# Kernel tuning notes

Hardware: AMD Instinct MI355X
Metric: run time of the kernel (lower is better)

The kernel has to match this reference:

```python
import jax, jax.numpy as jnp
from jax import lax
import numpy as np

NDIM = 256
BATCH = 65536
NROT = NDIM * (NDIM - 1) // 2  # comb(ndim, 2) = 32640


def _givens_mat(rots, ii, jj, ndim):
    """Product G_last @ ... @ G_1 of Givens rotations in combinations order.

    Left-multiplying by G(i, j, theta) only modifies rows i and j, so we apply
    each rotation as a rank-2 row update instead of a full matmul (same math
    as the original `plane_rot_mat @ mat` loop).
    """
    def step(mat, carry):
        i, j, th = carry
        c = jnp.cos(th)
        s = jnp.sin(th)
        ri = mat[i]
        rj = mat[j]
        mat = mat.at[i].set(c * ri - s * rj)
        mat = mat.at[j].set(s * ri + c * rj)
        return mat, None

    mat0 = jnp.eye(ndim, dtype=jnp.complex64)
    mat, _ = lax.scan(step, mat0, (ii, jj, rots))
    return mat


def setup_inputs() -> dict:
    key = jax.random.key(0)
    k1, k2, k3, k4 = jax.random.split(key, 4)
    x = jax.random.normal(k1, (BATCH, NDIM), dtype=jnp.float32)
    rots1 = 0.1 * jax.random.normal(k2, (NROT,), dtype=jnp.float32)
    phases = 0.1 * jax.random.normal(k3, (NDIM,), dtype=jnp.float32)
    rots2 = 0.1 * jax.random.normal(k4, (NROT,), dtype=jnp.float32)
    return {"x": x, "rots1": rots1, "phases": phases, "rots2": rots2}


def reference(x, rots1, phases, rots2):
    ndim = x.shape[1]
    # np.triu_indices(ndim, 1) enumerates (i, j) pairs in the same row-major
    # order as itertools.combinations(range(ndim), 2).
    ii_np, jj_np = np.triu_indices(ndim, k=1)
    ii = jnp.asarray(ii_np, dtype=jnp.int32)
    jj = jnp.asarray(jj_np, dtype=jnp.int32)

    # vector_norm: row-wise L2 normalization
    xn = x / jnp.linalg.norm(x, axis=1, keepdims=True)
    xc = xn.astype(jnp.complex64)

    # rot1: y = x @ M1.T with M1 = G_last @ ... @ G_1
    M1 = _givens_mat(rots1, ii, jj, ndim)
    y = xc @ M1.T

    # phase_transforms: x @ diag(exp(i*phases)) == elementwise phase multiply
    y = y * jnp.exp(1j * phases)

    # rot2
    M2 = _givens_mat(rots2, ii, jj, ndim)
    y = y @ M2.T

    # measure: |.|^2
    return jnp.abs(y) ** 2
```

## Files before the change

kernel.cpp:

```cpp
#include <hip/hip_runtime.h>
#include <stdint.h>
#include <math.h>

#define NDIM 256
#define BATCH 65536
#define NROT 32640

typedef float  f32x4 __attribute__((ext_vector_type(4)));
typedef short  s16x8 __attribute__((ext_vector_type(8)));
typedef unsigned int u32x4 __attribute__((ext_vector_type(4)));
typedef unsigned int u32x2 __attribute__((ext_vector_type(2)));

static __device__ __forceinline__ unsigned short f2bf(float f) {
    unsigned int u = __float_as_uint(f);
    u += 0x7fffu + ((u >> 16) & 1u);
    return (unsigned short)(u >> 16);
}
static __device__ __forceinline__ float bf2f(unsigned short h) {
    return __uint_as_float(((unsigned)h) << 16);
}

static __device__ __forceinline__ void split4(f32x4 v, u32x2* hi, u32x2* lo) {
    unsigned short h[4], l[4];
    #pragma unroll
    for (int i = 0; i < 4; i++) {
        h[i] = f2bf(v[i]);
        l[i] = f2bf(v[i] - bf2f(h[i]));
    }
    *hi = (u32x2){ (unsigned)h[0] | ((unsigned)h[1] << 16),
                   (unsigned)h[2] | ((unsigned)h[3] << 16) };
    *lo = (u32x2){ (unsigned)l[0] | ((unsigned)l[1] << 16),
                   (unsigned)l[2] | ((unsigned)l[3] << 16) };
}
static __device__ __forceinline__ void split8(const float* v, u32x4* hi, u32x4* lo) {
    unsigned short h[8], l[8];
    #pragma unroll
    for (int i = 0; i < 8; i++) {
        h[i] = f2bf(v[i]);
        l[i] = f2bf(v[i] - bf2f(h[i]));
    }
    *hi = (u32x4){ (unsigned)h[0] | ((unsigned)h[1] << 16),
                   (unsigned)h[2] | ((unsigned)h[3] << 16),
                   (unsigned)h[4] | ((unsigned)h[5] << 16),
                   (unsigned)h[6] | ((unsigned)h[7] << 16) };
    *lo = (u32x4){ (unsigned)l[0] | ((unsigned)l[1] << 16),
                   (unsigned)l[2] | ((unsigned)l[3] << 16),
                   (unsigned)l[4] | ((unsigned)l[5] << 16),
                   (unsigned)l[6] | ((unsigned)l[7] << 16) };
}

static __device__ __forceinline__ int sweep_bound(int k, int pblk) {
    int target = k * (NROT / pblk);
    int best = 0, bd = 0x7fffffff;
    for (int i = 0; i <= 256; i += 4) {
        int pre = i * 255 - (i * (i - 1)) / 2;
        int d = pre - target; d = (d < 0) ? -d : d;
        if (d < bd) { bd = d; best = i; }
    }
    return best;
}

__global__ __launch_bounds__(256) void k_cs(const float* __restrict__ r1,
                                            const float* __restrict__ r2,
                                            float2* __restrict__ cs) {
    int i = blockIdx.x * 256 + threadIdx.x;
    float th = (i < NROT) ? r1[i] : r2[i - NROT];
    float sv, cv; sincosf(th, &sv, &cv);
    cs[i] = make_float2(cv, sv);
}

__global__ __launch_bounds__(64) void k_blocks(const float2* __restrict__ cs,
                                               float* __restrict__ bmats, int pblk) {
    __shared__ float colb[264 * 64];
    __shared__ float2 csb[256 * 4];
    __shared__ float2 tri[24 * 6];

    const int t = threadIdx.x;
    const int bid = blockIdx.x;
    const int chunk = bid & 3;
    const int b = (bid >> 2) % pblk;
    const int set = (bid >> 2) / pblk;
    const int col0 = chunk * 64;
    const float2* cst = cs + (size_t)set * NROT;

    const int s0 = sweep_bound(b, pblk);
    const int s1 = sweep_bound(b + 1, pblk);
    const int ngroups = (s1 - s0) >> 2;

    {
        const f32x4 z = {0.f, 0.f, 0.f, 0.f};
        #pragma unroll 11
        for (int q = 0; q < 66; q++)
            *(f32x4*)&colb[(q * 64 + t) * 4] = z;
        colb[(col0 + t) * 64 + t] = 1.0f;
    }

    for (int k = t; k < ngroups * 6; k += 64) {
        int g = k / 6, q = k - g * 6;
        int a  = (q < 3) ? 0 : ((q < 5) ? 1 : 2);
        int bb = (q < 3) ? (q + 1) : ((q < 5) ? (q - 1) : 3);
        int m0 = s0 + g * 4;
        int m = m0 + a;
        int base = m * 255 - (m * (m - 1)) / 2;
        tri[k] = cst[base - m - 1 + m0 + bb];
    }

    float2 gv[16];
    {
        const int m0g = s0;
        int offg[4];
        #pragma unroll
        for (int a = 0; a < 4; a++) {
            int m = m0g + a;
            offg[a] = m * 255 - (m * (m - 1)) / 2 - m - 1;
        }
        #pragma unroll
        for (int it = 0; it < 16; it++) {
            int k = t + it * 64;
            int jj = k >> 2, a = k & 3;
            int j = m0g + 4 + jj;
            gv[it] = (j < 256) ? cst[offg[a] + j] : make_float2(1.f, 0.f);
        }
        #pragma unroll
        for (int it = 0; it < 16; it++)
            csb[t + it * 64] = gv[it];
    }

    for (int g = 0; g < ngroups; g++) {
        const int m0 = s0 + g * 4;
        const int n_j = 252 - m0;
        const int n_p = (n_j > 0) ? ((n_j + 7) & ~7) : 0;
        const float* csbuf = (const float*)&csb[0];

        const bool have_next = (g + 1 < ngroups);
        if (have_next) {
            const int m0g = m0 + 4;
            int offg[4];
            #pragma unroll
            for (int a = 0; a < 4; a++) {
                int m = m0g + a;
                offg[a] = m * 255 - (m * (m - 1)) / 2 - m - 1;
            }
            #pragma unroll
            for (int it = 0; it < 16; it++) {
                int k = t + it * 64;
                int jj = k >> 2, a = k & 3;
                int j = m0g + 4 + jj;
                gv[it] = (j < 256) ? cst[offg[a] + j] : make_float2(1.f, 0.f);
            }
        }

        float u0 = colb[(m0 + 0) * 64 + t];
        float u1 = colb[(m0 + 1) * 64 + t];
        float u2 = colb[(m0 + 2) * 64 + t];
        float u3 = colb[(m0 + 3) * 64 + t];

        {
            float2 cv; float nr;
            cv = tri[g * 6 + 0]; nr = cv.y * u0 + cv.x * u1; u0 = cv.x * u0 - cv.y * u1; u1 = nr;
            cv = tri[g * 6 + 1]; nr = cv.y * u0 + cv.x * u2; u0 = cv.x * u0 - cv.y * u2; u2 = nr;
            cv = tri[g * 6 + 2]; nr = cv.y * u0 + cv.x * u3; u0 = cv.x * u0 - cv.y * u3; u3 = nr;
            cv = tri[g * 6 + 3]; nr = cv.y * u1 + cv.x * u2; u1 = cv.x * u1 - cv.y * u2; u2 = nr;
            cv = tri[g * 6 + 4]; nr = cv.y * u1 + cv.x * u3; u1 = cv.x * u1 - cv.y * u3; u3 = nr;
            cv = tri[g * 6 + 5]; nr = cv.y * u2 + cv.x * u3; u2 = cv.x * u2 - cv.y * u3; u3 = nr;
        }

        if (n_p > 0) {
            float rbuf[8];
            f32x4 abuf[8][2];
            #pragma unroll
            for (int p = 0; p < 8; p++) {
                rbuf[p] = colb[(m0 + 4 + p) * 64 + t];
                abuf[p][0] = *(const f32x4*)&csbuf[p * 8 + 0];
                abuf[p][1] = *(const f32x4*)&csbuf[p * 8 + 4];
            }
            for (int c = 0; c < n_p; c += 8) {
                #pragma unroll
                for (int p = 0; p < 8; p++) {
                    const int j = m0 + 4 + c + p;
                    float r = rbuf[p];
                    f32x4 A01 = abuf[p][0], A23 = abuf[p][1];
                    int jn = j + 8; jn = (jn < 263) ? jn : 263;
                    int cn = c + p + 8; cn = (cn < n_p) ? cn : (n_p - 1);
                    rbuf[p] = colb[jn * 64 + t];
                    abuf[p][0] = *(const f32x4*)&csbuf[cn * 8 + 0];
                    abuf[p][1] = *(const f32x4*)&csbuf[cn * 8 + 4];
                    float nr;
                    nr = A01[1] * u0 + A01[0] * r; u0 = A01[0] * u0 - A01[1] * r; r = nr;
                    nr = A01[3] * u1 + A01[2] * r; u1 = A01[2] * u1 - A01[3] * r; r = nr;
                    nr = A23[1] * u2 + A23[0] * r; u2 = A23[0] * u2 - A23[1] * r; r = nr;
                    nr = A23[3] * u3 + A23[2] * r; u3 = A23[2] * u3 - A23[3] * r; r = nr;
                    colb[j * 64 + t] = r;
                }
            }
        }
        colb[(m0 + 0) * 64 + t] = u0;
        colb[(m0 + 1) * 64 + t] = u1;
        colb[(m0 + 2) * 64 + t] = u2;
        colb[(m0 + 3) * 64 + t] = u3;

        if (have_next) {
            #pragma unroll
            for (int it = 0; it < 16; it++)
                csb[t + it * 64] = gv[it];
        }
    }

    float* outm = bmats + (size_t)(set * pblk + b) * 65536;
    for (int r = 0; r < 256; r++)
        outm[(size_t)r * 256 + col0 + t] = colb[r * 64 + t];
}

static __device__ __forceinline__ void xnorm_item(const float* __restrict__ xg,
                                                  unsigned short* __restrict__ xbf,
                                                  int id, int tid) {
    const int w = tid >> 6, lane = tid & 63;
    const int r0 = id * 64;
    #pragma unroll 2
    for (int p = 0; p < 16; p++) {
        int row = r0 + p * 4 + w;
        f32x4 v = *(const f32x4*)&xg[(size_t)row * 256 + lane * 4];
        float s = v[0] * v[0] + v[1] * v[1] + v[2] * v[2] + v[3] * v[3];
        #pragma unroll
        for (int off = 32; off; off >>= 1) s += __shfl_xor(s, off, 64);
        float sc = 1.0f / sqrtf(s);
        unsigned short h0 = f2bf(v[0] * sc), h1 = f2bf(v[1] * sc);
        unsigned short h2 = f2bf(v[2] * sc), h3 = f2bf(v[3] * sc);
        u32x2 pk = { (unsigned)h0 | ((unsigned)h1 << 16),
                     (unsigned)h2 | ((unsigned)h3 << 16) };
        *(u32x2*)&xbf[(size_t)row * 256 + lane * 4] = pk;
    }
}

#define TB 2560

static __device__ __forceinline__ void tile_issueA(const float* __restrict__ Am,
                                                   int tr, int kb, int tid,
                                                   f32x4 va[2]) {
    #pragma unroll
    for (int it = 0; it < 2; it++) {
        int flat = tid + it * 256;
        int r = flat >> 3, c4 = flat & 7;
        va[it] = *(const f32x4*)&Am[(size_t)(tr * 64 + r) * 256 + kb * 32 + c4 * 4];
    }
}
static __device__ __forceinline__ void tile_issueB(const float* __restrict__ Bm,
                                                   int tc, int kb, int bn, int bkq,
                                                   float vb[8]) {
    #pragma unroll
    for (int i = 0; i < 8; i++)
        vb[i] = Bm[(size_t)(kb * 32 + bkq * 8 + i) * 256 + tc * 64 + bn];
}
static __device__ __forceinline__ void tile_commit(unsigned short* __restrict__ Ahi,
                                                   unsigned short* __restrict__ Alo,
                                                   unsigned short* __restrict__ Bhi,
                                                   unsigned short* __restrict__ Blo,
                                                   int tid, int bn, int bkq,
                                                   const f32x4 va[2], const float vb[8]) {
    #pragma unroll
    for (int it = 0; it < 2; it++) {
        int flat = tid + it * 256;
        int r = flat >> 3, c4 = flat & 7;
        u32x2 hi, lo; split4(va[it], &hi, &lo);
        *(u32x2*)&Ahi[r * 40 + c4 * 4] = hi;
        *(u32x2*)&Alo[r * 40 + c4 * 4] = lo;
    }
    u32x4 hi8, lo8; split8(vb, &hi8, &lo8);
    *(u32x4*)&Bhi[bn * 40 + bkq * 8] = hi8;
    *(u32x4*)&Blo[bn * 40 + bkq * 8] = lo8;
}
static __device__ __forceinline__ void tile_mfma(const unsigned short* __restrict__ Ahi,
                                                 const unsigned short* __restrict__ Alo,
                                                 const unsigned short* __restrict__ Bhi,
                                                 const unsigned short* __restrict__ Blo,
                                                 int mh, int nh, int l15, int lq,
                                                 f32x4 acc[2][2]) {
    s16x8 ah[2], al[2], bh[2], bl[2];
    #pragma unroll
    for (int tm = 0; tm < 2; tm++) {
        ah[tm] = *(const s16x8*)&Ahi[(mh + tm * 16 + l15) * 40 + lq * 8];
        al[tm] = *(const s16x8*)&Alo[(mh + tm * 16 + l15) * 40 + lq * 8];
    }
    #pragma unroll
    for (int tn = 0; tn < 2; tn++) {
        bh[tn] = *(const s16x8*)&Bhi[(nh + tn * 16 + l15) * 40 + lq * 8];
        bl[tn] = *(const s16x8*)&Blo[(nh + tn * 16 + l15) * 40 + lq * 8];
    }
    #pragma unroll
    for (int tm = 0; tm < 2; tm++)
        #pragma unroll
        for (int tn = 0; tn < 2; tn++) {
            acc[tm][tn] = __builtin_amdgcn_mfma_f32_16x16x32_bf16(ah[tm], bh[tn], acc[tm][tn], 0, 0, 0);
            acc[tm][tn] = __builtin_amdgcn_mfma_f32_16x16x32_bf16(ah[tm], bl[tn], acc[tm][tn], 0, 0, 0);
            acc[tm][tn] = __builtin_amdgcn_mfma_f32_16x16x32_bf16(al[tm], bh[tn], acc[tm][tn], 0, 0, 0);
        }
}

static __device__ void combine_tile(const float* __restrict__ src,
                                    float* __restrict__ dst,
                                    int half, int pblk, int bx, int by, int tid,
                                    unsigned short* Ahi, unsigned short* Alo,
                                    unsigned short* Bhi, unsigned short* Blo) {
    const int set = by / half, pidx = by % half;
    const int stride = pblk / (2 * half);
    const int s0A = sweep_bound((2 * pidx + 1) * stride, pblk);
    const float* Am = src + (size_t)(set * 2 * half + 2 * pidx + 1) * 65536;
    const float* Bm = src + (size_t)(set * 2 * half + 2 * pidx) * 65536;
    float* Dm = dst + (size_t)(set * half + pidx) * 65536;
    const int tr = bx >> 2, tc = bx & 3;

    if (tr * 64 + 64 <= s0A) {
        #pragma unroll
        for (int it = 0; it < 4; it++) {
            int flat = tid + it * 256;
            int r = flat >> 4, c4 = flat & 15;
            size_t idx = (size_t)(tr * 64 + r) * 256 + tc * 64 + c4 * 4;
            *(f32x4*)&Dm[idx] = *(const f32x4*)&Bm[idx];
        }
        return;
    }
    const int kb0 = (tr * 64 >= s0A) ? (s0A >> 5) : 0;

    const int lane = tid & 63, w = tid >> 6;
    const int mh = (w >> 1) * 32, nh = (w & 1) * 32;
    const int l15 = lane & 15, lq = lane >> 4;
    const int bn = tid & 63, bkq = tid >> 6;

    f32x4 acc[2][2];
    #pragma unroll
    for (int i = 0; i < 2; i++)
        #pragma unroll
        for (int j = 0; j < 2; j++) acc[i][j] = (f32x4){0.f, 0.f, 0.f, 0.f};

    f32x4 vaE[2], vaO[2]; float vbE[8], vbO[8];
    tile_issueA(Am, tr, kb0, tid, vaE);
    tile_issueB(Bm, tc, kb0, bn, bkq, vbE);
    if (kb0 + 1 < 8) {
        tile_issueA(Am, tr, kb0 + 1, tid, vaO);
        tile_issueB(Bm, tc, kb0 + 1, bn, bkq, vbO);
    }
    tile_commit(Ahi, Alo, Bhi, Blo, tid, bn, bkq, vaE, vbE);
    __syncthreads();

    for (int kb = kb0; kb < 8; kb++) {
        const int cur = (kb - kb0) & 1;
        if (cur == 0) {
            if (kb + 2 < 8) {
                tile_issueA(Am, tr, kb + 2, tid, vaE);
                tile_issueB(Bm, tc, kb + 2, bn, bkq, vbE);
            }
            if (kb + 1 < 8)
                tile_commit(Ahi + TB, Alo + TB, Bhi + TB, Blo + TB,
                            tid, bn, bkq, vaO, vbO);
            tile_mfma(Ahi, Alo, Bhi, Blo, mh, nh, l15, lq, acc);
        } else {
            if (kb + 2 < 8) {
                tile_issueA(Am, tr, kb + 2, tid, vaO);
                tile_issueB(Bm, tc, kb + 2, bn, bkq, vbO);
            }
            if (kb + 1 < 8)
                tile_commit(Ahi, Alo, Bhi, Blo, tid, bn, bkq, vaE, vbE);
            tile_mfma(Ahi + TB, Alo + TB, Bhi + TB, Blo + TB, mh, nh, l15, lq, acc);
        }
        __syncthreads();
    }
    #pragma unroll
    for (int tm = 0; tm < 2; tm++)
        #pragma unroll
        for (int tn = 0; tn < 2; tn++)
            #pragma unroll
            for (int r = 0; r < 4; r++)
                Dm[(size_t)(tr * 64 + mh + tm * 16 + lq * 4 + r) * 256
                   + tc * 64 + nh + tn * 16 + l15] = acc[tm][tn][r];
}

static __device__ void abt_tile(const float* __restrict__ mats,
                                const float* __restrict__ phases,
                                unsigned short* __restrict__ abtp,
                                int bx, int v, int tid,
                                unsigned short* Ahi, unsigned short* Alo,
                                unsigned short* Bhi, unsigned short* Blo) {
    const float* Am = mats + 65536;
    const float* Bm = mats;
    const int tr = bx >> 2, tc = bx & 3;

    const int lane = tid & 63, w = tid >> 6;
    const int mh = (w >> 1) * 32, nh = (w & 1) * 32;
    const int l15 = lane & 15, lq = lane >> 4;
    const int bn = tid & 63, bkq = tid >> 6;

    f32x4 acc[2][2];
    #pragma unroll
    for (int i = 0; i < 2; i++)
        #pragma unroll
        for (int j = 0; j < 2; j++) acc[i][j] = (f32x4){0.f, 0.f, 0.f, 0.f};

    auto issueBs = [&](int kb, float vb[8]) {
        #pragma unroll
        for (int i = 0; i < 8; i++) {
            int kg = kb * 32 + bkq * 8 + i;
            float ph = phases[kg];
            float sc = v ? sinf(ph) : cosf(ph);
            vb[i] = Bm[(size_t)kg * 256 + tc * 64 + bn] * sc;
        }
    };

    f32x4 vaE[2], vaO[2]; float vbE[8], vbO[8];
    tile_issueA(Am, tr, 0, tid, vaE); issueBs(0, vbE);
    tile_issueA(Am, tr, 1, tid, vaO); issueBs(1, vbO);
    tile_commit(Ahi, Alo, Bhi, Blo, tid, bn, bkq, vaE, vbE);
    __syncthreads();

    for (int kb = 0; kb < 8; kb++) {
        const int cur = kb & 1;
        if (cur == 0) {
            if (kb + 2 < 8) { tile_issueA(Am, tr, kb + 2, tid, vaE); issueBs(kb + 2, vbE); }
            if (kb + 1 < 8)
                tile_commit(Ahi + TB, Alo + TB, Bhi + TB, Blo + TB,
                            tid, bn, bkq, vaO, vbO);
            tile_mfma(Ahi, Alo, Bhi, Blo, mh, nh, l15, lq, acc);
        } else {
            if (kb + 2 < 8) { tile_issueA(Am, tr, kb + 2, tid, vaO); issueBs(kb + 2, vbO); }
            if (kb + 1 < 8)
                tile_commit(Ahi, Alo, Bhi, Blo, tid, bn, bkq, vaE, vbE);
            tile_mfma(Ahi + TB, Alo + TB, Bhi + TB, Blo + TB, mh, nh, l15, lq, acc);
        }
        __syncthreads();
    }
    #pragma unroll
    for (int tm = 0; tm < 2; tm++)
        #pragma unroll
        for (int tn = 0; tn < 2; tn++)
            #pragma unroll
            for (int r = 0; r < 4; r++)
                abtp[(size_t)(v * 256 + tr * 64 + mh + tm * 16 + lq * 4 + r) * 256
                     + tc * 64 + nh + tn * 16 + l15] = f2bf(acc[tm][tn][r]);
}

__global__ __launch_bounds__(256) void k_combine(const float* __restrict__ src,
                                                 float* __restrict__ dst,
                                                 int half, int pblk,
                                                 const float* __restrict__ xg,
                                                 unsigned short* __restrict__ xbf) {
    __shared__ unsigned short Ahi[2 * TB], Alo[2 * TB], Bhi[2 * TB], Blo[2 * TB];
    const int by = blockIdx.y, tid = threadIdx.x;
    if (by >= 2 * half) {
        xnorm_item(xg, xbf, (by - 2 * half) * 16 + blockIdx.x, tid);
        return;
    }
    combine_tile(src, dst, half, pblk, blockIdx.x, by, tid, Ahi, Alo, Bhi, Blo);
}

__global__ __launch_bounds__(256) void k_abt(const float* __restrict__ mats,
                                             const float* __restrict__ phases,
                                             unsigned short* __restrict__ abtp) {
    __shared__ unsigned short Ahi[2 * TB], Alo[2 * TB], Bhi[2 * TB], Blo[2 * TB];
    abt_tile(mats, phases, abtp, blockIdx.x, blockIdx.y, threadIdx.x,
             Ahi, Alo, Bhi, Blo);
}

__global__ __launch_bounds__(256) void k_norm(const float* __restrict__ x,
                                              float* __restrict__ invn) {
    const int row = blockIdx.x * 4 + (threadIdx.x >> 6);
    const int lane = threadIdx.x & 63;
    f32x4 v = *(const f32x4*)&x[(size_t)row * 256 + lane * 4];
    float s = v[0] * v[0] + v[1] * v[1] + v[2] * v[2] + v[3] * v[3];
    for (int off = 32; off; off >>= 1) s += __shfl_xor(s, off, 64);
    if (lane == 0) invn[row] = 1.0f / sqrtf(s);
}

#define BKP 136
__global__ __launch_bounds__(256) void k_gemm_bf(const unsigned short* __restrict__ xbf,
                                                 const unsigned short* __restrict__ abt,
                                                 float* __restrict__ out) {
    __shared__ unsigned short As[128 * BKP];
    __shared__ unsigned short Bs[128 * BKP];
    const int tid = threadIdx.x;
    const int l  = blockIdx.y * 4 + blockIdx.x;
    const int L  = (l & 7) * 256 + (l >> 3);
    const int cb = L & 3;
    const int rb = L >> 2;
    const int lane = tid & 63, w = tid >> 6;

    f32x4 acc[16];
    #pragma unroll
    for (int i = 0; i < 16; i++) acc[i] = (f32x4){0.f, 0.f, 0.f, 0.f};

    int rA[8], cA[8], grB[8];
    #pragma unroll
    for (int it = 0; it < 8; it++) {
        int flat = tid + it * 256;
        rA[it] = flat >> 4; cA[it] = flat & 15;
        int r = rA[it];
        grB[it] = (r < 64) ? (cb * 64 + r) : (256 + cb * 64 + (r - 64));
    }

    u32x4 pa[8], pb[8];
    #pragma unroll
    for (int it = 0; it < 8; it++) {
        pa[it] = *(const u32x4*)&xbf[(size_t)(rb * 128 + rA[it]) * 256 + cA[it] * 8];
        pb[it] = *(const u32x4*)&abt[(size_t)grB[it] * 256 + cA[it] * 8];
    }
    #pragma unroll
    for (int it = 0; it < 8; it++) {
        *(u32x4*)&As[rA[it] * BKP + cA[it] * 8] = pa[it];
        *(u32x4*)&Bs[rA[it] * BKP + cA[it] * 8] = pb[it];
    }
    __syncthreads();
    #pragma unroll
    for (int it = 0; it < 8; it++) {
        pa[it] = *(const u32x4*)&xbf[(size_t)(rb * 128 + rA[it]) * 256 + 128 + cA[it] * 8];
        pb[it] = *(const u32x4*)&abt[(size_t)grB[it] * 256 + 128 + cA[it] * 8];
    }

    auto compute = [&]() {
        #pragma unroll
        for (int ks = 0; ks < 4; ks++) {
            const int k0 = ks * 32 + (lane >> 4) * 8;
            s16x8 a[2], b[8];
            #pragma unroll
            for (int tm = 0; tm < 2; tm++)
                a[tm] = *(const s16x8*)&As[(w * 32 + tm * 16 + (lane & 15)) * BKP + k0];
            #pragma unroll
            for (int tn = 0; tn < 8; tn++)
                b[tn] = *(const s16x8*)&Bs[(tn * 16 + (lane & 15)) * BKP + k0];
            #pragma unroll
            for (int tm = 0; tm < 2; tm++)
                #pragma unroll
                for (int tn = 0; tn < 8; tn++)
                    acc[tm * 8 + tn] = __builtin_amdgcn_mfma_f32_16x16x32_bf16(
                        a[tm], b[tn], acc[tm * 8 + tn], 0, 0, 0);
        }
    };
    compute();
    __syncthreads();
    #pragma unroll
    for (int it = 0; it < 8; it++) {
        *(u32x4*)&As[rA[it] * BKP + cA[it] * 8] = pa[it];
        *(u32x4*)&Bs[rA[it] * BKP + cA[it] * 8] = pb[it];
    }
    __syncthreads();
    compute();

    const int qr = lane >> 4, c = lane & 15;
    #pragma unroll
    for (int tm = 0; tm < 2; tm++) {
        #pragma unroll
        for (int tn = 0; tn < 4; tn++) {
            f32x4 p = acc[tm * 8 + tn];
            f32x4 q = acc[tm * 8 + tn + 4];
            #pragma unroll
            for (int r = 0; r < 4; r++) {
                int m = w * 32 + tm * 16 + qr * 4 + r;
                out[(size_t)(rb * 128 + m) * 256 + cb * 64 + tn * 16 + c] =
                    p[r] * p[r] + q[r] * q[r];
            }
        }
    }
}

__global__ __launch_bounds__(256) void k_gemm_f32(const float* __restrict__ x,
                                                  const unsigned short* __restrict__ abt,
                                                  const float* __restrict__ invn,
                                                  float* __restrict__ out) {
    __shared__ unsigned short As[128 * BKP];
    __shared__ unsigned short Bs[128 * BKP];
    const int tid = threadIdx.x;
    const int l  = blockIdx.y * 4 + blockIdx.x;
    const int L  = (l & 7) * 256 + (l >> 3);
    const int cb = L & 3;
    const int rb = L >> 2;
    const int lane = tid & 63, w = tid >> 6;

    f32x4 acc[16];
    #pragma unroll
    for (int i = 0; i < 16; i++) acc[i] = (f32x4){0.f, 0.f, 0.f, 0.f};

    for (int kb = 0; kb < 2; kb++) {
        __syncthreads();
        #pragma unroll
        for (int it = 0; it < 16; it++) {
            int flat = tid + it * 256;
            int r = flat >> 5, c4 = flat & 31;
            f32x4 v = *(const f32x4*)&x[(size_t)(rb * 128 + r) * 256 + kb * 128 + c4 * 4];
            float sc = invn[rb * 128 + r];
            v[0] *= sc; v[1] *= sc; v[2] *= sc; v[3] *= sc;
            unsigned short h0 = f2bf(v[0]), h1 = f2bf(v[1]);
            unsigned short h2 = f2bf(v[2]), h3 = f2bf(v[3]);
            u32x2 pk = { (unsigned)h0 | ((unsigned)h1 << 16),
                         (unsigned)h2 | ((unsigned)h3 << 16) };
            *(u32x2*)&As[r * BKP + c4 * 4] = pk;
        }
        #pragma unroll
        for (int it = 0; it < 8; it++) {
            int flat = tid + it * 256;
            int r = flat >> 4, c8 = flat & 15;
            int gr = (r < 64) ? (cb * 64 + r) : (256 + cb * 64 + (r - 64));
            u32x4 vv = *(const u32x4*)&abt[(size_t)gr * 256 + kb * 128 + c8 * 8];
            *(u32x4*)&Bs[r * BKP + c8 * 8] = vv;
        }
        __syncthreads();
        #pragma unroll
        for (int ks = 0; ks < 4; ks++) {
            const int k0 = ks * 32 + (lane >> 4) * 8;
            s16x8 a[2], b[8];
            #pragma unroll
            for (int tm = 0; tm < 2; tm++)
                a[tm] = *(const s16x8*)&As[(w * 32 + tm * 16 + (lane & 15)) * BKP + k0];
            #pragma unroll
            for (int tn = 0; tn < 8; tn++)
                b[tn] = *(const s16x8*)&Bs[(tn * 16 + (lane & 15)) * BKP + k0];
            #pragma unroll
            for (int tm = 0; tm < 2; tm++)
                #pragma unroll
                for (int tn = 0; tn < 8; tn++)
                    acc[tm * 8 + tn] = __builtin_amdgcn_mfma_f32_16x16x32_bf16(
                        a[tm], b[tn], acc[tm * 8 + tn], 0, 0, 0);
        }
    }

    const int qr = lane >> 4, c = lane & 15;
    #pragma unroll
    for (int tm = 0; tm < 2; tm++) {
        #pragma unroll
        for (int tn = 0; tn < 4; tn++) {
            f32x4 p = acc[tm * 8 + tn];
            f32x4 q = acc[tm * 8 + tn + 4];
            #pragma unroll
            for (int r = 0; r < 4; r++) {
                int m = w * 32 + tm * 16 + qr * 4 + r;
                out[(size_t)(rb * 128 + m) * 256 + cb * 64 + tn * 16 + c] =
                    p[r] * p[r] + q[r] * q[r];
            }
        }
    }
}

extern "C" void kernel_launch(void* const* d_in, const int* in_sizes, int n_in,
                              void* d_out, int out_size, void* d_ws, size_t ws_size,
                              hipStream_t stream) {
    (void)in_sizes; (void)n_in; (void)out_size;
    const float* x      = (const float*)d_in[0];
    const float* rots1  = (const float*)d_in[1];
    const float* phases = (const float*)d_in[2];
    const float* rots2  = (const float*)d_in[3];
    float* out = (float*)d_out;
    char* ws = (char*)d_ws;

    const size_t MAT = 262144;
    int pblk = 64;
    while (pblk > 16 &&
           (size_t)3 * pblk * MAT + 2 * MAT + (size_t)BATCH * 512 > ws_size)
        pblk >>= 1;
    const size_t offA   = 0;
    const size_t offB   = offA + (size_t)2 * pblk * MAT;
    const size_t offABT = offB + (size_t)pblk * MAT;
    const size_t offINV = offABT + MAT;
    const size_t offXBF = offINV + MAT;
    const bool use_xbf = (offXBF + (size_t)BATCH * 512) <= ws_size;

    float*          A    = (float*)(ws + offA);
    float*          B    = (float*)(ws + offB);
    unsigned short* abt  = (unsigned short*)(ws + offABT);
    float*          invn = (float*)(ws + offINV);
    unsigned short* xbf  = (unsigned short*)(ws + offXBF);
    float2*         cs   = (float2*)(ws + offB);

    k_cs<<<(2 * NROT) / 256, 256, 0, stream>>>(rots1, rots2, cs);
    k_blocks<<<8 * pblk, 64, 0, stream>>>(cs, A, pblk);

    float* srcp = A; float* dstp = B;
    bool first = true;
    for (int half = pblk / 2; half >= 1; half >>= 1) {
        const int xny = (first && use_xbf) ? 64 : 0;
        k_combine<<<dim3(16, 2 * half + xny), 256, 0, stream>>>(srcp, dstp, half,
                                                                pblk, x, xbf);
        float* tmp = srcp; srcp = dstp; dstp = tmp;
        first = false;
    }
    k_abt<<<dim3(16, 2), 256, 0, stream>>>(srcp, phases, abt);

    if (use_xbf) {
        k_gemm_bf<<<dim3(4, BATCH / 128), 256, 0, stream>>>(xbf, abt, out);
    } else {
        k_norm<<<BATCH / 4, 256, 0, stream>>>(x, invn);
        k_gemm_f32<<<dim3(4, BATCH / 128), 256, 0, stream>>>(x, abt, invn, out);
    }
}
```

Measured before the change: 284.6 us.

## Single-buffer LDS tiles in combine/abt GEMMs and swizzle B tile layout

Replaces the double-buffered LDS staging in the combine and abt tile GEMMs with a single buffer. Each k-step now commits the prefetched registers, syncs, issues the next global loads, runs the MFMAs and syncs again. This halves the shared memory per block, which can raise occupancy, at the cost of an extra barrier per iteration and less overlap between LDS writes and MFMA work. It also XOR-swizzles the B tile's 8-element slots by row to reduce LDS bank conflicts on the 16-byte reads and writes.

```diff
diff --git a/kernel.cpp b/kernel.cpp
--- a/kernel.cpp
+++ b/kernel.cpp
@@ -234,6 +234,10 @@
 
 #define TB 2560
 
+static __device__ __forceinline__ int bslot(int row, int s) {
+    return row * 40 + ((s ^ ((row >> 3) & 3)) << 3);
+}
+
 static __device__ __forceinline__ void tile_issueA(const float* __restrict__ Am,
                                                    int tr, int kb, int tid,
                                                    f32x4 va[2]) {
@@ -266,8 +270,8 @@
         *(u32x2*)&Alo[r * 40 + c4 * 4] = lo;
     }
     u32x4 hi8, lo8; split8(vb, &hi8, &lo8);
-    *(u32x4*)&Bhi[bn * 40 + bkq * 8] = hi8;
-    *(u32x4*)&Blo[bn * 40 + bkq * 8] = lo8;
+    *(u32x4*)&Bhi[bslot(bn, bkq)] = hi8;
+    *(u32x4*)&Blo[bslot(bn, bkq)] = lo8;
 }
 static __device__ __forceinline__ void tile_mfma(const unsigned short* __restrict__ Ahi,
                                                  const unsigned short* __restrict__ Alo,
@@ -283,8 +287,8 @@
     }
     #pragma unroll
     for (int tn = 0; tn < 2; tn++) {
-        bh[tn] = *(const s16x8*)&Bhi[(nh + tn * 16 + l15) * 40 + lq * 8];
-        bl[tn] = *(const s16x8*)&Blo[(nh + tn * 16 + l15) * 40 + lq * 8];
+        bh[tn] = *(const s16x8*)&Bhi[bslot(nh + tn * 16 + l15, lq)];
+        bl[tn] = *(const s16x8*)&Blo[bslot(nh + tn * 16 + l15, lq)];
     }
     #pragma unroll
     for (int tm = 0; tm < 2; tm++)
@@ -339,29 +343,25 @@
         tile_issueA(Am, tr, kb0 + 1, tid, vaO);
         tile_issueB(Bm, tc, kb0 + 1, bn, bkq, vbO);
     }
-    tile_commit(Ahi, Alo, Bhi, Blo, tid, bn, bkq, vaE, vbE);
-    __syncthreads();
 
     for (int kb = kb0; kb < 8; kb++) {
         const int cur = (kb - kb0) & 1;
         if (cur == 0) {
+            tile_commit(Ahi, Alo, Bhi, Blo, tid, bn, bkq, vaE, vbE);
+            __syncthreads();
             if (kb + 2 < 8) {
                 tile_issueA(Am, tr, kb + 2, tid, vaE);
                 tile_issueB(Bm, tc, kb + 2, bn, bkq, vbE);
             }
-            if (kb + 1 < 8)
-                tile_commit(Ahi + TB, Alo + TB, Bhi + TB, Blo + TB,
-                            tid, bn, bkq, vaO, vbO);
-            tile_mfma(Ahi, Alo, Bhi, Blo, mh, nh, l15, lq, acc);
         } else {
+            tile_commit(Ahi, Alo, Bhi, Blo, tid, bn, bkq, vaO, vbO);
+            __syncthreads();
             if (kb + 2 < 8) {
                 tile_issueA(Am, tr, kb + 2, tid, vaO);
                 tile_issueB(Bm, tc, kb + 2, bn, bkq, vbO);
             }
-            if (kb + 1 < 8)
-                tile_commit(Ahi, Alo, Bhi, Blo, tid, bn, bkq, vaE, vbE);
-            tile_mfma(Ahi + TB, Alo + TB, Bhi + TB, Blo + TB, mh, nh, l15, lq, acc);
-        }
+        }
+        tile_mfma(Ahi, Alo, Bhi, Blo, mh, nh, l15, lq, acc);
         __syncthreads();
     }
     #pragma unroll
@@ -408,23 +408,19 @@
     f32x4 vaE[2], vaO[2]; float vbE[8], vbO[8];
     tile_issueA(Am, tr, 0, tid, vaE); issueBs(0, vbE);
     tile_issueA(Am, tr, 1, tid, vaO); issueBs(1, vbO);
-    tile_commit(Ahi, Alo, Bhi, Blo, tid, bn, bkq, vaE, vbE);
-    __syncthreads();
 
     for (int kb = 0; kb < 8; kb++) {
         const int cur = kb & 1;
         if (cur == 0) {
+            tile_commit(Ahi, Alo, Bhi, Blo, tid, bn, bkq, vaE, vbE);
+            __syncthreads();
             if (kb + 2 < 8) { tile_issueA(Am, tr, kb + 2, tid, vaE); issueBs(kb + 2, vbE); }
-            if (kb + 1 < 8)
-                tile_commit(Ahi + TB, Alo + TB, Bhi + TB, Blo + TB,
-                            tid, bn, bkq, vaO, vbO);
-            tile_mfma(Ahi, Alo, Bhi, Blo, mh, nh, l15, lq, acc);
         } else {
+            tile_commit(Ahi, Alo, Bhi, Blo, tid, bn, bkq, vaO, vbO);
+            __syncthreads();
             if (kb + 2 < 8) { tile_issueA(Am, tr, kb + 2, tid, vaO); issueBs(kb + 2, vbO); }
-            if (kb + 1 < 8)
-                tile_commit(Ahi, Alo, Bhi, Blo, tid, bn, bkq, vaE, vbE);
-            tile_mfma(Ahi + TB, Alo + TB, Bhi + TB, Blo + TB, mh, nh, l15, lq, acc);
-        }
+        }
+        tile_mfma(Ahi, Alo, Bhi, Blo, mh, nh, l15, lq, acc);
         __syncthreads();
     }
     #pragma unroll
@@ -442,7 +438,7 @@
                                                  int half, int pblk,
                                                  const float* __restrict__ xg,
                                                  unsigned short* __restrict__ xbf) {
-    __shared__ unsigned short Ahi[2 * TB], Alo[2 * TB], Bhi[2 * TB], Blo[2 * TB];
+    __shared__ unsigned short Ahi[TB], Alo[TB], Bhi[TB], Blo[TB];
     const int by = blockIdx.y, tid = threadIdx.x;
     if (by >= 2 * half) {
         xnorm_item(xg, xbf, (by - 2 * half) * 16 + blockIdx.x, tid);
@@ -454,7 +450,7 @@
 __global__ __launch_bounds__(256) void k_abt(const float* __restrict__ mats,
                                              const float* __restrict__ phases,
                                              unsigned short* __restrict__ abtp) {
-    __shared__ unsigned short Ahi[2 * TB], Alo[2 * TB], Bhi[2 * TB], Blo[2 * TB];
+    __shared__ unsigned short Ahi[TB], Alo[TB], Bhi[TB], Blo[TB];
     abt_tile(mats, phases, abtp, blockIdx.x, blockIdx.y, threadIdx.x,
              Ahi, Alo, Bhi, Blo);
 }
```

Result: no change. 279.8 us (-1.7%).
